# Optimization experiments

Measured on AMD Instinct MI355X. Metric: run time of the kernel, lower is better.

The kernel has to match this reference:

```python
import jax, jax.numpy as jnp
import numpy as np

NUM_HEADS = 16
BIG_NEG = -1e9  # additive mask value for padded keys (fp32)


def setup_inputs() -> dict:
    key = jax.random.key(0)
    ks = jax.random.split(key, 12)
    T, S, B, E = 2048, 2048, 2, 1024
    bound = np.sqrt(6.0 / (E + E))  # xavier_uniform for square E x E weights
    inp = {
        'query': jax.random.normal(ks[0], (T, B, E), jnp.float32),
        'key': jax.random.normal(ks[1], (S, B, E), jnp.float32),
        'value': jax.random.normal(ks[2], (S, B, E), jnp.float32),
        'attn_mask': jax.random.normal(ks[3], (T, S), jnp.float32) * 0.1,
        'key_padding_mask': jnp.zeros((B, S), dtype=bool),
        'Wq': jax.random.uniform(ks[4], (E, E), jnp.float32, -bound, bound),
        'bq': jnp.zeros((E,), jnp.float32),
        'Wk': jax.random.uniform(ks[5], (E, E), jnp.float32, -bound, bound),
        'bk': jnp.zeros((E,), jnp.float32),
        'Wv': jax.random.uniform(ks[6], (E, E), jnp.float32, -bound, bound),
        'bv': jnp.zeros((E,), jnp.float32),
        'Wo': jax.random.uniform(ks[7], (E, E), jnp.float32, -bound, bound),
        'bo': jnp.zeros((E,), jnp.float32),
    }
    return inp


def reference(query, key, value, attn_mask, key_padding_mask,
              Wq, bq, Wk, bk, Wv, bv, Wo, bo):
    T, B, E = query.shape
    S = key.shape[0]
    H = NUM_HEADS
    d = E // H
    scale = 1.0 / jnp.sqrt(jnp.asarray(d, query.dtype))

    # projections (nn.Linear: x @ W.T + b), then split heads
    q = (query @ Wq.T + bq).reshape(T, B, H, d) * scale  # [T,B,H,d]
    k = (key @ Wk.T + bk).reshape(S, B, H, d)            # [S,B,H,d]
    v = (value @ Wv.T + bv).reshape(S, B, H, d)          # [S,B,H,d]

    # QK^T scores: [B,H,T,S]
    scores = jnp.einsum('tbhd,sbhd->bhts', q, k)

    # merge masks: additive attn_mask + key_padding_mask (True -> -inf)
    merged = attn_mask[None, None, :, :] + jnp.where(
        key_padding_mask[:, None, None, :], BIG_NEG, 0.0).astype(scores.dtype)
    scores = scores + merged

    attn = jax.nn.softmax(scores, axis=-1)  # dropout p=0 -> identity

    out = jnp.einsum('bhts,sbhd->tbhd', attn, v).reshape(T, B, E)
    return out @ Wo.T + bo  # [T,B,E]
```

## Files before the change

kernel.cpp:

```cpp
#include <hip/hip_runtime.h>
#include <hip/hip_bf16.h>

typedef unsigned short u16;
typedef __attribute__((ext_vector_type(8))) short bf16x8;
typedef __attribute__((ext_vector_type(4))) float f32x4;

#define T_DIM 2048
#define S_DIM 2048
#define B_DIM 2
#define E_DIM 1024
#define H_DIM 16
#define D_HEAD 64
#define NTOK 4096

#if __has_builtin(__builtin_amdgcn_exp2f)
#define EXP2F(x) __builtin_amdgcn_exp2f(x)
#else
#define EXP2F(x) exp2f(x)
#endif

__device__ __forceinline__ float bf2f(u16 u) {
  union { unsigned int i; float f; } v; v.i = ((unsigned int)u) << 16; return v.f;
}
__device__ __forceinline__ u16 f2bf(float f) {
  union { float f; unsigned int i; } v; v.f = f;
  unsigned int r = v.i + 0x7fffu + ((v.i >> 16) & 1u);
  return (u16)(r >> 16);
}
__device__ __forceinline__ unsigned pk2(float a, float b) {
  return (unsigned)f2bf(a) | ((unsigned)f2bf(b) << 16);
}
__device__ __forceinline__ uint4 loadA8(const void* A, size_t base, int bf) {
  if (bf) return *(const uint4*)&((const u16*)A)[base];
  const float* af = (const float*)A + base;
  uint4 r;
  r.x = pk2(af[0], af[1]); r.y = pk2(af[2], af[3]);
  r.z = pk2(af[4], af[5]); r.w = pk2(af[6], af[7]);
  return r;
}

__global__ void detect_dtype(const u16* q, int* flag) {
  int lane = threadIdx.x;
  float v = bf2f(q[2 * lane]);
  bool ok = (v < 16.f) && (v > -16.f);
  unsigned long long b = __ballot(ok);
  if (lane == 0) *flag = (b == ~0ull) ? 1 : 0;
}

__global__ void prep_params(const void* Wq, const void* Wk, const void* Wv, const void* Wo,
                            const void* bq, const void* bk, const void* bv, const void* bo,
                            u16* wqkv, u16* wo, float* b3, float* bof,
                            const int* flag) {
  const int bf = *flag;
  const int W = E_DIM * E_DIM;
  int idx = blockIdx.x * 256 + threadIdx.x;
  if (idx < 4 * W) {
    int which = idx / W, i = idx - which * W;
    const void* src = which == 0 ? Wq : which == 1 ? Wk : which == 2 ? Wv : Wo;
    float v = bf ? bf2f(((const u16*)src)[i]) : ((const float*)src)[i];
    if (which == 0) v *= 0.125f;
    if (which < 3) wqkv[idx] = f2bf(v);
    else           wo[i] = f2bf(v);
  } else {
    int j = idx - 4 * W;
    if (j < 4 * E_DIM) {
      int which = j / E_DIM, i = j - which * E_DIM;
      const void* src = which == 0 ? bq : which == 1 ? bk : which == 2 ? bv : bo;
      float v = bf ? bf2f(((const u16*)src)[i]) : ((const float*)src)[i];
      if (which == 0) v *= 0.125f;
      if (which < 3) b3[j] = v;
      else           bof[i] = v;
    }
  }
}

__global__ void prep_mask(const void* mask, const unsigned char* kpm,
                          u16* Mc, const int* flag) {
  const float L2E = 1.44269504f;
  const int bf = *flag;
  size_t e8 = ((size_t)blockIdx.x * 256 + threadIdx.x) * 8;
  int b = (int)(e8 / ((size_t)T_DIM * S_DIM));
  size_t rem = e8 - (size_t)b * T_DIM * S_DIM;
  int t = (int)(rem / S_DIM), s = (int)(rem - (size_t)t * S_DIM);
  const unsigned char* kb = &kpm[(size_t)b * S_DIM + s];
  uint4 o;
  if (bf) {
    const u16* m8 = &((const u16*)mask)[(size_t)t * S_DIM + s];
    o.x = pk2((bf2f(m8[0]) + (kb[0] ? -1e9f : 0.f)) * L2E,
              (bf2f(m8[1]) + (kb[1] ? -1e9f : 0.f)) * L2E);
    o.y = pk2((bf2f(m8[2]) + (kb[2] ? -1e9f : 0.f)) * L2E,
              (bf2f(m8[3]) + (kb[3] ? -1e9f : 0.f)) * L2E);
    o.z = pk2((bf2f(m8[4]) + (kb[4] ? -1e9f : 0.f)) * L2E,
              (bf2f(m8[5]) + (kb[5] ? -1e9f : 0.f)) * L2E);
    o.w = pk2((bf2f(m8[6]) + (kb[6] ? -1e9f : 0.f)) * L2E,
              (bf2f(m8[7]) + (kb[7] ? -1e9f : 0.f)) * L2E);
  } else {
    const float* mf = (const float*)mask + (size_t)t * S_DIM + s;
    o.x = pk2((mf[0] + (kb[0] ? -1e9f : 0.f)) * L2E,
              (mf[1] + (kb[1] ? -1e9f : 0.f)) * L2E);
    o.y = pk2((mf[2] + (kb[2] ? -1e9f : 0.f)) * L2E,
              (mf[3] + (kb[3] ? -1e9f : 0.f)) * L2E);
    o.z = pk2((mf[4] + (kb[4] ? -1e9f : 0.f)) * L2E,
              (mf[5] + (kb[5] ? -1e9f : 0.f)) * L2E);
    o.w = pk2((mf[6] + (kb[6] ? -1e9f : 0.f)) * L2E,
              (mf[7] + (kb[7] ? -1e9f : 0.f)) * L2E);
  }
  *(uint4*)&Mc[e8] = o;
}

__launch_bounds__(256)
__global__ void transpose_v(const u16* __restrict__ vp, u16* __restrict__ vt) {
  __shared__ unsigned int t[64 * 65];
  const int tid = threadIdx.x;
  const int s0 = blockIdx.x * 64;
  const int bh = blockIdx.y;
  const int b = bh / H_DIM, h = bh % H_DIM;
  {
    int sr = tid >> 2, cq = (tid & 3) * 16;
    const u16* src = &vp[((size_t)(s0 + sr) * B_DIM + b) * E_DIM + h * 64 + cq];
#pragma unroll
    for (int j = 0; j < 16; j++) t[(cq + j) * 65 + sr] = src[j];
  }
  __syncthreads();
  {
    int d = tid >> 2, sq = (tid & 3) * 16;
    u16* dst = &vt[((size_t)bh * 64 + d) * S_DIM + s0 + sq];
    uint4 o0, o1;
    o0.x = (t[d*65+sq+0] & 0xffffu) | (t[d*65+sq+1] << 16);
    o0.y = (t[d*65+sq+2] & 0xffffu) | (t[d*65+sq+3] << 16);
    o0.z = (t[d*65+sq+4] & 0xffffu) | (t[d*65+sq+5] << 16);
    o0.w = (t[d*65+sq+6] & 0xffffu) | (t[d*65+sq+7] << 16);
    o1.x = (t[d*65+sq+8] & 0xffffu) | (t[d*65+sq+9] << 16);
    o1.y = (t[d*65+sq+10] & 0xffffu) | (t[d*65+sq+11] << 16);
    o1.z = (t[d*65+sq+12] & 0xffffu) | (t[d*65+sq+13] << 16);
    o1.w = (t[d*65+sq+14] & 0xffffu) | (t[d*65+sq+15] << 16);
    *(uint4*)&dst[0] = o0;
    *(uint4*)&dst[8] = o1;
  }
}

__launch_bounds__(256, 2)
__global__ void gemm_qkv(const void* __restrict__ Qi, const void* __restrict__ Ki,
                         const void* __restrict__ Vi, const u16* __restrict__ W3,
                         const float* __restrict__ b3,
                         u16* __restrict__ qp, u16* __restrict__ kp, u16* __restrict__ vp,
                         const int* __restrict__ flag) {
  __shared__ alignas(16) u16 As[128 * 72];
  __shared__ alignas(16) u16 Bs[128 * 72];
  const int bf = *flag;
  const int tid = threadIdx.x;
  const int wave = tid >> 6, lane = tid & 63;
  const int g = lane >> 4, c = lane & 15;
  const int wy = wave >> 1, wx = wave & 1;
  const int which = blockIdx.x >> 3;
  const void* A = which == 0 ? Qi : which == 1 ? Ki : Vi;
  u16* dst = which == 0 ? qp : which == 1 ? kp : vp;
  const int m0 = blockIdx.y * 128, n0 = blockIdx.x * 128;
  const int K = E_DIM;
  const int rr = tid >> 3, oo = (tid & 7) * 8;

  uint4 pa0, pa1, pa2, pa3, pb0, pb1, pb2, pb3;
  pa0 = loadA8(A, (size_t)(m0 + rr)      * K + oo, bf);
  pa1 = loadA8(A, (size_t)(m0 + rr + 32) * K + oo, bf);
  pa2 = loadA8(A, (size_t)(m0 + rr + 64) * K + oo, bf);
  pa3 = loadA8(A, (size_t)(m0 + rr + 96) * K + oo, bf);
  pb0 = *(const uint4*)&W3[(size_t)(n0 + rr)      * K + oo];
  pb1 = *(const uint4*)&W3[(size_t)(n0 + rr + 32) * K + oo];
  pb2 = *(const uint4*)&W3[(size_t)(n0 + rr + 64) * K + oo];
  pb3 = *(const uint4*)&W3[(size_t)(n0 + rr + 96) * K + oo];

  f32x4 acc[4][4] = {};
  for (int kc = 0; kc < K; kc += 64) {
    *(uint4*)&As[(rr)      * 72 + oo] = pa0;
    *(uint4*)&As[(rr + 32) * 72 + oo] = pa1;
    *(uint4*)&As[(rr + 64) * 72 + oo] = pa2;
    *(uint4*)&As[(rr + 96) * 72 + oo] = pa3;
    *(uint4*)&Bs[(rr)      * 72 + oo] = pb0;
    *(uint4*)&Bs[(rr + 32) * 72 + oo] = pb1;
    *(uint4*)&Bs[(rr + 64) * 72 + oo] = pb2;
    *(uint4*)&Bs[(rr + 96) * 72 + oo] = pb3;
    __syncthreads();
    if (kc + 64 < K) {
      int k2 = kc + 64;
      pa0 = loadA8(A, (size_t)(m0 + rr)      * K + k2 + oo, bf);
      pa1 = loadA8(A, (size_t)(m0 + rr + 32) * K + k2 + oo, bf);
      pa2 = loadA8(A, (size_t)(m0 + rr + 64) * K + k2 + oo, bf);
      pa3 = loadA8(A, (size_t)(m0 + rr + 96) * K + k2 + oo, bf);
      pb0 = *(const uint4*)&W3[(size_t)(n0 + rr)      * K + k2 + oo];
      pb1 = *(const uint4*)&W3[(size_t)(n0 + rr + 32) * K + k2 + oo];
      pb2 = *(const uint4*)&W3[(size_t)(n0 + rr + 64) * K + k2 + oo];
      pb3 = *(const uint4*)&W3[(size_t)(n0 + rr + 96) * K + k2 + oo];
    }
#pragma unroll
    for (int ks = 0; ks < 2; ks++) {
      bf16x8 av0 = *(const bf16x8*)&As[(wy * 64 + 0 * 16 + c) * 72 + ks * 32 + g * 8];
      bf16x8 av1 = *(const bf16x8*)&As[(wy * 64 + 1 * 16 + c) * 72 + ks * 32 + g * 8];
      bf16x8 av2 = *(const bf16x8*)&As[(wy * 64 + 2 * 16 + c) * 72 + ks * 32 + g * 8];
      bf16x8 av3 = *(const bf16x8*)&As[(wy * 64 + 3 * 16 + c) * 72 + ks * 32 + g * 8];
      bf16x8 bv0 = *(const bf16x8*)&Bs[(wx * 64 + 0 * 16 + c) * 72 + ks * 32 + g * 8];
      bf16x8 bv1 = *(const bf16x8*)&Bs[(wx * 64 + 1 * 16 + c) * 72 + ks * 32 + g * 8];
      bf16x8 bv2 = *(const bf16x8*)&Bs[(wx * 64 + 2 * 16 + c) * 72 + ks * 32 + g * 8];
      bf16x8 bv3 = *(const bf16x8*)&Bs[(wx * 64 + 3 * 16 + c) * 72 + ks * 32 + g * 8];
      acc[0][0] = __builtin_amdgcn_mfma_f32_16x16x32_bf16(av0, bv0, acc[0][0], 0, 0, 0);
      acc[0][1] = __builtin_amdgcn_mfma_f32_16x16x32_bf16(av0, bv1, acc[0][1], 0, 0, 0);
      acc[0][2] = __builtin_amdgcn_mfma_f32_16x16x32_bf16(av0, bv2, acc[0][2], 0, 0, 0);
      acc[0][3] = __builtin_amdgcn_mfma_f32_16x16x32_bf16(av0, bv3, acc[0][3], 0, 0, 0);
      acc[1][0] = __builtin_amdgcn_mfma_f32_16x16x32_bf16(av1, bv0, acc[1][0], 0, 0, 0);
      acc[1][1] = __builtin_amdgcn_mfma_f32_16x16x32_bf16(av1, bv1, acc[1][1], 0, 0, 0);
      acc[1][2] = __builtin_amdgcn_mfma_f32_16x16x32_bf16(av1, bv2, acc[1][2], 0, 0, 0);
      acc[1][3] = __builtin_amdgcn_mfma_f32_16x16x32_bf16(av1, bv3, acc[1][3], 0, 0, 0);
      acc[2][0] = __builtin_amdgcn_mfma_f32_16x16x32_bf16(av2, bv0, acc[2][0], 0, 0, 0);
      acc[2][1] = __builtin_amdgcn_mfma_f32_16x16x32_bf16(av2, bv1, acc[2][1], 0, 0, 0);
      acc[2][2] = __builtin_amdgcn_mfma_f32_16x16x32_bf16(av2, bv2, acc[2][2], 0, 0, 0);
      acc[2][3] = __builtin_amdgcn_mfma_f32_16x16x32_bf16(av2, bv3, acc[2][3], 0, 0, 0);
      acc[3][0] = __builtin_amdgcn_mfma_f32_16x16x32_bf16(av3, bv0, acc[3][0], 0, 0, 0);
      acc[3][1] = __builtin_amdgcn_mfma_f32_16x16x32_bf16(av3, bv1, acc[3][1], 0, 0, 0);
      acc[3][2] = __builtin_amdgcn_mfma_f32_16x16x32_bf16(av3, bv2, acc[3][2], 0, 0, 0);
      acc[3][3] = __builtin_amdgcn_mfma_f32_16x16x32_bf16(av3, bv3, acc[3][3], 0, 0, 0);
    }
    __syncthreads();
  }
#pragma unroll
  for (int mi = 0; mi < 4; mi++)
#pragma unroll
    for (int ni = 0; ni < 4; ni++)
#pragma unroll
      for (int r = 0; r < 4; r++) {
        int row = m0 + wy * 64 + mi * 16 + g * 4 + r;
        int col = n0 + wx * 64 + ni * 16 + c;
        int inner = col & (E_DIM - 1);
        dst[(size_t)row * E_DIM + inner] = f2bf(acc[mi][ni][r] + b3[col]);
      }
}

__launch_bounds__(256, 2)
__global__ void gemm_o(const u16* __restrict__ A, const u16* __restrict__ Bw,
                       const float* __restrict__ bias, void* __restrict__ C,
                       int out_f32) {
  __shared__ alignas(16) u16 As[64 * 72];
  __shared__ alignas(16) u16 Bs[128 * 72];
  const int tid = threadIdx.x;
  const int wave = tid >> 6, lane = tid & 63;
  const int g = lane >> 4, c = lane & 15;
  const int wy = wave >> 1, wx = wave & 1;
  const int m0 = blockIdx.y * 64, n0 = blockIdx.x * 128;
  const int K = E_DIM, N = E_DIM;
  const int rr = tid >> 3, oo = (tid & 7) * 8;

  uint4 pa0, pa1, pb0, pb1, pb2, pb3;
  pa0 = *(const uint4*)&A[(size_t)(m0 + rr)      * K + oo];
  pa1 = *(const uint4*)&A[(size_t)(m0 + rr + 32) * K + oo];
  pb0 = *(const uint4*)&Bw[(size_t)(n0 + rr)      * K + oo];
  pb1 = *(const uint4*)&Bw[(size_t)(n0 + rr + 32) * K + oo];
  pb2 = *(const uint4*)&Bw[(size_t)(n0 + rr + 64) * K + oo];
  pb3 = *(const uint4*)&Bw[(size_t)(n0 + rr + 96) * K + oo];

  f32x4 acc[2][4] = {};
  for (int kc = 0; kc < K; kc += 64) {
    *(uint4*)&As[(rr)      * 72 + oo] = pa0;
    *(uint4*)&As[(rr + 32) * 72 + oo] = pa1;
    *(uint4*)&Bs[(rr)      * 72 + oo] = pb0;
    *(uint4*)&Bs[(rr + 32) * 72 + oo] = pb1;
    *(uint4*)&Bs[(rr + 64) * 72 + oo] = pb2;
    *(uint4*)&Bs[(rr + 96) * 72 + oo] = pb3;
    __syncthreads();
    if (kc + 64 < K) {
      int k2 = kc + 64;
      pa0 = *(const uint4*)&A[(size_t)(m0 + rr)      * K + k2 + oo];
      pa1 = *(const uint4*)&A[(size_t)(m0 + rr + 32) * K + k2 + oo];
      pb0 = *(const uint4*)&Bw[(size_t)(n0 + rr)      * K + k2 + oo];
      pb1 = *(const uint4*)&Bw[(size_t)(n0 + rr + 32) * K + k2 + oo];
      pb2 = *(const uint4*)&Bw[(size_t)(n0 + rr + 64) * K + k2 + oo];
      pb3 = *(const uint4*)&Bw[(size_t)(n0 + rr + 96) * K + k2 + oo];
    }
#pragma unroll
    for (int ks = 0; ks < 2; ks++) {
      bf16x8 av0 = *(const bf16x8*)&As[(wy * 32 + 0 * 16 + c) * 72 + ks * 32 + g * 8];
      bf16x8 av1 = *(const bf16x8*)&As[(wy * 32 + 1 * 16 + c) * 72 + ks * 32 + g * 8];
      bf16x8 bv0 = *(const bf16x8*)&Bs[(wx * 64 + 0 * 16 + c) * 72 + ks * 32 + g * 8];
      bf16x8 bv1 = *(const bf16x8*)&Bs[(wx * 64 + 1 * 16 + c) * 72 + ks * 32 + g * 8];
      bf16x8 bv2 = *(const bf16x8*)&Bs[(wx * 64 + 2 * 16 + c) * 72 + ks * 32 + g * 8];
      bf16x8 bv3 = *(const bf16x8*)&Bs[(wx * 64 + 3 * 16 + c) * 72 + ks * 32 + g * 8];
      acc[0][0] = __builtin_amdgcn_mfma_f32_16x16x32_bf16(av0, bv0, acc[0][0], 0, 0, 0);
      acc[0][1] = __builtin_amdgcn_mfma_f32_16x16x32_bf16(av0, bv1, acc[0][1], 0, 0, 0);
      acc[0][2] = __builtin_amdgcn_mfma_f32_16x16x32_bf16(av0, bv2, acc[0][2], 0, 0, 0);
      acc[0][3] = __builtin_amdgcn_mfma_f32_16x16x32_bf16(av0, bv3, acc[0][3], 0, 0, 0);
      acc[1][0] = __builtin_amdgcn_mfma_f32_16x16x32_bf16(av1, bv0, acc[1][0], 0, 0, 0);
      acc[1][1] = __builtin_amdgcn_mfma_f32_16x16x32_bf16(av1, bv1, acc[1][1], 0, 0, 0);
      acc[1][2] = __builtin_amdgcn_mfma_f32_16x16x32_bf16(av1, bv2, acc[1][2], 0, 0, 0);
      acc[1][3] = __builtin_amdgcn_mfma_f32_16x16x32_bf16(av1, bv3, acc[1][3], 0, 0, 0);
    }
    __syncthreads();
  }
#pragma unroll
  for (int mi = 0; mi < 2; mi++)
#pragma unroll
    for (int ni = 0; ni < 4; ni++)
#pragma unroll
      for (int r = 0; r < 4; r++) {
        int row = m0 + wy * 32 + mi * 16 + g * 4 + r;
        int col = n0 + wx * 64 + ni * 16 + c;
        float v = acc[mi][ni][r] + bias[col];
        size_t idx = (size_t)row * N + col;
        if (out_f32) ((float*)C)[idx] = v;
        else         ((u16*)C)[idx] = f2bf(v);
      }
}

__launch_bounds__(256, 4)
__global__ void flash_attn(const u16* __restrict__ Qb, const u16* __restrict__ Kb,
                           const u16* __restrict__ Vtg, const u16* __restrict__ Mc,
                           u16* __restrict__ ctx) {
  __shared__ alignas(16) u16 Ks[64 * 72];
  __shared__ alignas(16) u16 Vs[64 * 72];
  __shared__ alignas(16) u16 MP[64 * 72];
  const int tid = threadIdx.x;
  const int wave = tid >> 6, lane = tid & 63;
  const int g = lane >> 4, c = lane & 15;
  const int bh = blockIdx.x;
  const int t0 = blockIdx.y * 64;
  const int b = bh / H_DIM, h = bh % H_DIM;
  const size_t hoff = (size_t)h * D_HEAD;
  const float L2E = 1.44269504f;
  const u16* mc = &Mc[((size_t)b * T_DIM + t0) * S_DIM];
  const int rr = tid >> 3, oo = (tid & 7) * 8;

  *(uint4*)&Ks[(rr)      * 72 + oo] =
      *(const uint4*)&Qb[((size_t)(t0 + rr)      * B_DIM + b) * E_DIM + hoff + oo];
  *(uint4*)&Ks[(rr + 32) * 72 + oo] =
      *(const uint4*)&Qb[((size_t)(t0 + rr + 32) * B_DIM + b) * E_DIM + hoff + oo];
  __syncthreads();
  const int arow = wave * 16 + c;
  bf16x8 q0 = *(const bf16x8*)&Ks[arow * 72 + g * 8];
  bf16x8 q1 = *(const bf16x8*)&Ks[arow * 72 + 32 + g * 8];

  uint4 pk0, pk1, pv0, pv1, pm0, pm1;
  pk0 = *(const uint4*)&Kb[((size_t)(rr)      * B_DIM + b) * E_DIM + hoff + oo];
  pk1 = *(const uint4*)&Kb[((size_t)(rr + 32) * B_DIM + b) * E_DIM + hoff + oo];
  pv0 = *(const uint4*)&Vtg[((size_t)bh * 64 + rr)      * S_DIM + oo];
  pv1 = *(const uint4*)&Vtg[((size_t)bh * 64 + rr + 32) * S_DIM + oo];
  pm0 = *(const uint4*)&mc[(size_t)(rr)      * S_DIM + oo];
  pm1 = *(const uint4*)&mc[(size_t)(rr + 32) * S_DIM + oo];
  __syncthreads();

  f32x4 O[4] = {};
  float rs[4] = {0.f, 0.f, 0.f, 0.f};

  for (int s0 = 0; s0 < S_DIM; s0 += 64) {
    *(uint4*)&Ks[(rr)      * 72 + oo] = pk0;
    *(uint4*)&Ks[(rr + 32) * 72 + oo] = pk1;
    *(uint4*)&Vs[(rr)      * 72 + oo] = pv0;
    *(uint4*)&Vs[(rr + 32) * 72 + oo] = pv1;
    *(uint4*)&MP[(rr)      * 72 + oo] = pm0;
    *(uint4*)&MP[(rr + 32) * 72 + oo] = pm1;
    __syncthreads();
    if (s0 + 64 < S_DIM) {
      int s2 = s0 + 64;
      pk0 = *(const uint4*)&Kb[((size_t)(s2 + rr)      * B_DIM + b) * E_DIM + hoff + oo];
      pk1 = *(const uint4*)&Kb[((size_t)(s2 + rr + 32) * B_DIM + b) * E_DIM + hoff + oo];
      pv0 = *(const uint4*)&Vtg[((size_t)bh * 64 + rr)      * S_DIM + s2 + oo];
      pv1 = *(const uint4*)&Vtg[((size_t)bh * 64 + rr + 32) * S_DIM + s2 + oo];
      pm0 = *(const uint4*)&mc[(size_t)(rr)      * S_DIM + s2 + oo];
      pm1 = *(const uint4*)&mc[(size_t)(rr + 32) * S_DIM + s2 + oo];
    }

    f32x4 sc[4] = {};
#pragma unroll
    for (int n = 0; n < 4; n++) {
      bf16x8 k0 = *(const bf16x8*)&Ks[(n * 16 + c) * 72 + g * 8];
      bf16x8 k1 = *(const bf16x8*)&Ks[(n * 16 + c) * 72 + 32 + g * 8];
      sc[n] = __builtin_amdgcn_mfma_f32_16x16x32_bf16(q0, k0, sc[n], 0, 0, 0);
      sc[n] = __builtin_amdgcn_mfma_f32_16x16x32_bf16(q1, k1, sc[n], 0, 0, 0);
    }
#pragma unroll
    for (int n = 0; n < 4; n++)
#pragma unroll
      for (int r = 0; r < 4; r++) {
        int a = (wave * 16 + g * 4 + r) * 72 + n * 16 + c;
        float pval = EXP2F(fmaf(sc[n][r], L2E, bf2f(MP[a])));
        rs[r] += pval;
        MP[a] = f2bf(pval);
      }
    bf16x8 p0 = *(const bf16x8*)&MP[arow * 72 + g * 8];
    bf16x8 p1 = *(const bf16x8*)&MP[arow * 72 + 32 + g * 8];
#pragma unroll
    for (int n = 0; n < 4; n++) {
      bf16x8 v0 = *(const bf16x8*)&Vs[(n * 16 + c) * 72 + g * 8];
      bf16x8 v1 = *(const bf16x8*)&Vs[(n * 16 + c) * 72 + 32 + g * 8];
      O[n] = __builtin_amdgcn_mfma_f32_16x16x32_bf16(p0, v0, O[n], 0, 0, 0);
      O[n] = __builtin_amdgcn_mfma_f32_16x16x32_bf16(p1, v1, O[n], 0, 0, 0);
    }
    __syncthreads();
  }
#pragma unroll
  for (int r = 0; r < 4; r++) {
    float l = rs[r];
#pragma unroll
    for (int off = 1; off < 16; off <<= 1) l += __shfl_xor(l, off, 64);
    float rl = 1.f / l;
    int t = t0 + wave * 16 + g * 4 + r;
#pragma unroll
    for (int n = 0; n < 4; n++) {
      int dcol = n * 16 + c;
      ctx[((size_t)t * B_DIM + b) * E_DIM + hoff + dcol] = f2bf(O[n][r] * rl);
    }
  }
}

extern "C" void kernel_launch(void* const* d_in, const int* in_sizes, int n_in,
                              void* d_out, int out_size, void* d_ws, size_t ws_size,
                              hipStream_t stream) {
  const void* query = d_in[0];
  const void* key   = d_in[1];
  const void* value = d_in[2];
  const void* amask = d_in[3];
  const unsigned char* kpm = (const unsigned char*)d_in[4];
  const void* Wq = d_in[5];  const void* bq = d_in[6];
  const void* Wk = d_in[7];  const void* bk = d_in[8];
  const void* Wv = d_in[9];  const void* bv = d_in[10];
  const void* Wo = d_in[11]; const void* bo = d_in[12];

  int out_f32 = 0;
  {
    hipDeviceptr_t base = nullptr; size_t sz = 0;
    if (hipMemGetAddressRange(&base, &sz, (hipDeviceptr_t)d_out) == hipSuccess && sz) {
      size_t avail = sz - (size_t)((char*)d_out - (char*)base);
      size_t need_f32 = (size_t)out_size * 4;
      if (avail >= need_f32 && avail <= need_f32 + need_f32 / 2) out_f32 = 1;
    }
  }

  char* ws = (char*)d_ws;
  size_t off = 0;
  auto alloc = [&](size_t bytes) {
    void* p = ws + off;
    off += (bytes + 255) & ~(size_t)255;
    return p;
  };
  int*   flag = (int*)  alloc(256);
  u16*   qp   = (u16*)  alloc((size_t)NTOK * E_DIM * 2);
  u16*   kp   = (u16*)  alloc((size_t)NTOK * E_DIM * 2);
  u16*   vp   = (u16*)  alloc((size_t)NTOK * E_DIM * 2);
  u16*   vt   = (u16*)  alloc((size_t)NTOK * E_DIM * 2);
  u16*   Mcb  = (u16*)  alloc((size_t)B_DIM * T_DIM * S_DIM * 2);
  u16*   wqkv = (u16*)  alloc((size_t)3 * E_DIM * E_DIM * 2);
  u16*   wo   = (u16*)  alloc((size_t)E_DIM * E_DIM * 2);
  float* b3   = (float*)alloc(3 * E_DIM * 4);
  float* bof  = (float*)alloc(E_DIM * 4);
  if (off > ws_size) return;

  detect_dtype<<<1, 64, 0, stream>>>((const u16*)query, flag);

  {
    int total = 4 * E_DIM * E_DIM + 4 * E_DIM;
    prep_params<<<(total + 255) / 256, 256, 0, stream>>>(
        Wq, Wk, Wv, Wo, bq, bk, bv, bo, wqkv, wo, b3, bof, flag);
  }
  {
    size_t total8 = (size_t)B_DIM * T_DIM * S_DIM / 8;
    prep_mask<<<(unsigned)(total8 / 256), 256, 0, stream>>>(amask, kpm, Mcb, flag);
  }

  gemm_qkv<<<dim3(3 * E_DIM / 128, NTOK / 128), 256, 0, stream>>>(
      query, key, value, wqkv, b3, qp, kp, vp, flag);

  transpose_v<<<dim3(S_DIM / 64, B_DIM * H_DIM), 256, 0, stream>>>(vp, vt);

  u16* ctx = vp;
  flash_attn<<<dim3(B_DIM * H_DIM, T_DIM / 64), 256, 0, stream>>>(qp, kp, vt, Mcb, ctx);

  gemm_o<<<dim3(E_DIM / 128, NTOK / 64), 256, 0, stream>>>(ctx, wo, bof, d_out, out_f32);
}
```

Measured before the change: 311.4 us.

## Split attention over key dimension per wave, keep P in registers, reduce O via LDS

Restructures the flash attention kernel so each wave owns a 16-key slice of every 64-key tile instead of 16 query rows. Scores are computed as K·Q^T, so the exponentiated probabilities stay in registers and feed the PV MFMA directly, with two key tiles processed per iteration. This removes the LDS round trip for the mask and P tiles. Partial output accumulators are summed across waves through LDS at the end, which raises register use (occupancy hint dropped from 4 to 3) and adds a cross-wave reduction step. Mask values are now read straight from global memory inside the softmax step.

Measured after the change: 442.2 us. +42.0%, slower.

```diff
diff --git a/kernel.cpp b/kernel.cpp
--- a/kernel.cpp
+++ b/kernel.cpp
@@ -29,6 +29,17 @@
 }
 __device__ __forceinline__ unsigned pk2(float a, float b) {
   return (unsigned)f2bf(a) | ((unsigned)f2bf(b) << 16);
+}
+__device__ __forceinline__ float bfu_lo(unsigned w) {
+  union { unsigned int i; float f; } v; v.i = w << 16; return v.f;
+}
+__device__ __forceinline__ float bfu_hi(unsigned w) {
+  union { unsigned int i; float f; } v; v.i = w & 0xffff0000u; return v.f;
+}
+__device__ __forceinline__ bf16x8 mk8(uint2 a, uint2 b) {
+  union { uint4 u; bf16x8 v; } x;
+  x.u = make_uint4(a.x, a.y, b.x, b.y);
+  return x.v;
 }
 __device__ __forceinline__ uint4 loadA8(const void* A, size_t base, int bf) {
   if (bf) return *(const uint4*)&((const u16*)A)[base];
@@ -307,13 +318,49 @@
       }
 }
 
-__launch_bounds__(256, 4)
+#define STAGE(VSB) do {                                                        \
+    *(uint4*)&Ks[(rr)      * 72 + oo] = pkA;                                   \
+    *(uint4*)&Ks[(rr + 32) * 72 + oo] = pkB;                                   \
+    *(uint4*)&(VSB)[(rr)      * 72 + oo] = pvA;                                \
+    *(uint4*)&(VSB)[(rr + 32) * 72 + oo] = pvB;                                \
+  } while (0)
+
+#define PREFETCH(S2) do {                                                      \
+    pkA = *(const uint4*)&Kb[((size_t)((S2) + rr)      * B_DIM + b) * E_DIM + hoff + oo]; \
+    pkB = *(const uint4*)&Kb[((size_t)((S2) + rr + 32) * B_DIM + b) * E_DIM + hoff + oo]; \
+    pvA = *(const uint4*)&Vtg[((size_t)bh * 64 + rr)      * S_DIM + (S2) + oo]; \
+    pvB = *(const uint4*)&Vtg[((size_t)bh * 64 + rr + 32) * S_DIM + (S2) + oo]; \
+  } while (0)
+
+#define QKSOFT(PB, S0) do {                                                    \
+    f32x4 sc[4] = {};                                                          \
+    bf16x8 kf0 = *(const bf16x8*)&Ks[w16c * 72 + g * 8];                       \
+    bf16x8 kf1 = *(const bf16x8*)&Ks[w16c * 72 + 32 + g * 8];                  \
+    _Pragma("unroll")                                                          \
+    for (int n = 0; n < 4; n++) {                                              \
+      sc[n] = __builtin_amdgcn_mfma_f32_16x16x32_bf16(kf0, q[n][0], sc[n], 0, 0, 0); \
+      sc[n] = __builtin_amdgcn_mfma_f32_16x16x32_bf16(kf1, q[n][1], sc[n], 0, 0, 0); \
+    }                                                                          \
+    _Pragma("unroll")                                                          \
+    for (int n = 0; n < 4; n++) {                                              \
+      uint2 mw = *(const uint2*)&mc[(size_t)(n * 16 + c) * S_DIM + (S0) + wS + g * 4]; \
+      float p0 = EXP2F(fmaf(sc[n][0], L2E, bfu_lo(mw.x)));                     \
+      float p1 = EXP2F(fmaf(sc[n][1], L2E, bfu_hi(mw.x)));                     \
+      float p2 = EXP2F(fmaf(sc[n][2], L2E, bfu_lo(mw.y)));                     \
+      float p3 = EXP2F(fmaf(sc[n][3], L2E, bfu_hi(mw.y)));                     \
+      rs[n] += (p0 + p1) + (p2 + p3);                                          \
+      PB[n] = make_uint2(pk2(p0, p1), pk2(p2, p3));                            \
+    }                                                                          \
+  } while (0)
+
+__launch_bounds__(256, 3)
 __global__ void flash_attn(const u16* __restrict__ Qb, const u16* __restrict__ Kb,
                            const u16* __restrict__ Vtg, const u16* __restrict__ Mc,
                            u16* __restrict__ ctx) {
-  __shared__ alignas(16) u16 Ks[64 * 72];
-  __shared__ alignas(16) u16 Vs[64 * 72];
-  __shared__ alignas(16) u16 MP[64 * 72];
+  __shared__ alignas(16) u16 SH[3 * 64 * 72];
+  u16* Ks  = SH;
+  u16* Vs0 = SH + 4608;
+  u16* Vs1 = SH + 2 * 4608;
   const int tid = threadIdx.x;
   const int wave = tid >> 6, lane = tid & 63;
   const int g = lane >> 4, c = lane & 15;
@@ -324,86 +371,85 @@
   const float L2E = 1.44269504f;
   const u16* mc = &Mc[((size_t)b * T_DIM + t0) * S_DIM];
   const int rr = tid >> 3, oo = (tid & 7) * 8;
+  const int w16c = wave * 16 + c;
+  const int wS   = wave * 16;
 
   *(uint4*)&Ks[(rr)      * 72 + oo] =
       *(const uint4*)&Qb[((size_t)(t0 + rr)      * B_DIM + b) * E_DIM + hoff + oo];
   *(uint4*)&Ks[(rr + 32) * 72 + oo] =
       *(const uint4*)&Qb[((size_t)(t0 + rr + 32) * B_DIM + b) * E_DIM + hoff + oo];
   __syncthreads();
-  const int arow = wave * 16 + c;
-  bf16x8 q0 = *(const bf16x8*)&Ks[arow * 72 + g * 8];
-  bf16x8 q1 = *(const bf16x8*)&Ks[arow * 72 + 32 + g * 8];
-
-  uint4 pk0, pk1, pv0, pv1, pm0, pm1;
-  pk0 = *(const uint4*)&Kb[((size_t)(rr)      * B_DIM + b) * E_DIM + hoff + oo];
-  pk1 = *(const uint4*)&Kb[((size_t)(rr + 32) * B_DIM + b) * E_DIM + hoff + oo];
-  pv0 = *(const uint4*)&Vtg[((size_t)bh * 64 + rr)      * S_DIM + oo];
-  pv1 = *(const uint4*)&Vtg[((size_t)bh * 64 + rr + 32) * S_DIM + oo];
-  pm0 = *(const uint4*)&mc[(size_t)(rr)      * S_DIM + oo];
-  pm1 = *(const uint4*)&mc[(size_t)(rr + 32) * S_DIM + oo];
+  bf16x8 q[4][2];
+#pragma unroll
+  for (int n = 0; n < 4; n++) {
+    q[n][0] = *(const bf16x8*)&Ks[(n * 16 + c) * 72 + g * 8];
+    q[n][1] = *(const bf16x8*)&Ks[(n * 16 + c) * 72 + 32 + g * 8];
+  }
+
+  uint4 pkA, pkB, pvA, pvB;
+  PREFETCH(0);
   __syncthreads();
 
-  f32x4 O[4] = {};
+  f32x4 o[4][4] = {};
   float rs[4] = {0.f, 0.f, 0.f, 0.f};
-
-  for (int s0 = 0; s0 < S_DIM; s0 += 64) {
-    *(uint4*)&Ks[(rr)      * 72 + oo] = pk0;
-    *(uint4*)&Ks[(rr + 32) * 72 + oo] = pk1;
-    *(uint4*)&Vs[(rr)      * 72 + oo] = pv0;
-    *(uint4*)&Vs[(rr + 32) * 72 + oo] = pv1;
-    *(uint4*)&MP[(rr)      * 72 + oo] = pm0;
-    *(uint4*)&MP[(rr + 32) * 72 + oo] = pm1;
-    __syncthreads();
-    if (s0 + 64 < S_DIM) {
-      int s2 = s0 + 64;
-      pk0 = *(const uint4*)&Kb[((size_t)(s2 + rr)      * B_DIM + b) * E_DIM + hoff + oo];
-      pk1 = *(const uint4*)&Kb[((size_t)(s2 + rr + 32) * B_DIM + b) * E_DIM + hoff + oo];
-      pv0 = *(const uint4*)&Vtg[((size_t)bh * 64 + rr)      * S_DIM + s2 + oo];
-      pv1 = *(const uint4*)&Vtg[((size_t)bh * 64 + rr + 32) * S_DIM + s2 + oo];
-      pm0 = *(const uint4*)&mc[(size_t)(rr)      * S_DIM + s2 + oo];
-      pm1 = *(const uint4*)&mc[(size_t)(rr + 32) * S_DIM + s2 + oo];
-    }
-
-    f32x4 sc[4] = {};
-#pragma unroll
-    for (int n = 0; n < 4; n++) {
-      bf16x8 k0 = *(const bf16x8*)&Ks[(n * 16 + c) * 72 + g * 8];
-      bf16x8 k1 = *(const bf16x8*)&Ks[(n * 16 + c) * 72 + 32 + g * 8];
-      sc[n] = __builtin_amdgcn_mfma_f32_16x16x32_bf16(q0, k0, sc[n], 0, 0, 0);
-      sc[n] = __builtin_amdgcn_mfma_f32_16x16x32_bf16(q1, k1, sc[n], 0, 0, 0);
-    }
+  uint2 pbA[4], pbB[4];
+
+  for (int s0 = 0; s0 < S_DIM; s0 += 128) {
+    STAGE(Vs0);
+    __syncthreads();
+    PREFETCH(s0 + 64);
+    QKSOFT(pbA, s0);
+    __syncthreads();
+    STAGE(Vs1);
+    __syncthreads();
+    if (s0 + 128 < S_DIM) PREFETCH(s0 + 128);
+    QKSOFT(pbB, s0 + 64);
+#pragma unroll
+    for (int m = 0; m < 4; m++) {
+      uint2 va0 = *(const uint2*)&Vs0[(m * 16 + c) * 72 + wS + g * 4];
+      uint2 vb0 = *(const uint2*)&Vs1[(m * 16 + c) * 72 + wS + g * 4];
+      bf16x8 va = mk8(va0, vb0);
+#pragma unroll
+      for (int n = 0; n < 4; n++)
+        o[m][n] = __builtin_amdgcn_mfma_f32_16x16x32_bf16(va, mk8(pbA[n], pbB[n]),
+                                                          o[m][n], 0, 0, 0);
+    }
+    __syncthreads();
+  }
+
+  float l[4];
+#pragma unroll
+  for (int n = 0; n < 4; n++) {
+    float x = rs[n];
+    x += __shfl_xor(x, 16, 64);
+    x += __shfl_xor(x, 32, 64);
+    l[n] = x;
+  }
+  float* R  = (float*)SH;
+  float* Rs = (float*)(SH + 2 * 4608);
+  if (lane < 16) {
+#pragma unroll
+    for (int n = 0; n < 4; n++) Rs[wave * 64 + n * 16 + c] = l[n];
+  }
+  const int tt = tid >> 2, d4 = (tid & 3) * 4;
+  u16* cp = &ctx[((size_t)(t0 + tt) * B_DIM + b) * E_DIM + hoff + d4];
+  float rl = 0.f;
+#pragma unroll
+  for (int m = 0; m < 4; m++) {
 #pragma unroll
     for (int n = 0; n < 4; n++)
-#pragma unroll
-      for (int r = 0; r < 4; r++) {
-        int a = (wave * 16 + g * 4 + r) * 72 + n * 16 + c;
-        float pval = EXP2F(fmaf(sc[n][r], L2E, bf2f(MP[a])));
-        rs[r] += pval;
-        MP[a] = f2bf(pval);
-      }
-    bf16x8 p0 = *(const bf16x8*)&MP[arow * 72 + g * 8];
-    bf16x8 p1 = *(const bf16x8*)&MP[arow * 72 + 32 + g * 8];
-#pragma unroll
-    for (int n = 0; n < 4; n++) {
-      bf16x8 v0 = *(const bf16x8*)&Vs[(n * 16 + c) * 72 + g * 8];
-      bf16x8 v1 = *(const bf16x8*)&Vs[(n * 16 + c) * 72 + 32 + g * 8];
-      O[n] = __builtin_amdgcn_mfma_f32_16x16x32_bf16(p0, v0, O[n], 0, 0, 0);
-      O[n] = __builtin_amdgcn_mfma_f32_16x16x32_bf16(p1, v1, O[n], 0, 0, 0);
-    }
-    __syncthreads();
-  }
-#pragma unroll
-  for (int r = 0; r < 4; r++) {
-    float l = rs[r];
-#pragma unroll
-    for (int off = 1; off < 16; off <<= 1) l += __shfl_xor(l, off, 64);
-    float rl = 1.f / l;
-    int t = t0 + wave * 16 + g * 4 + r;
-#pragma unroll
-    for (int n = 0; n < 4; n++) {
-      int dcol = n * 16 + c;
-      ctx[((size_t)t * B_DIM + b) * E_DIM + hoff + dcol] = f2bf(O[n][r] * rl);
-    }
+      *(f32x4*)&R[wave * 1024 + (n * 16 + c) * 16 + g * 4] = o[m][n];
+    __syncthreads();
+    if (m == 0)
+      rl = 1.f / (Rs[tt] + Rs[64 + tt] + Rs[128 + tt] + Rs[192 + tt]);
+    f32x4 v0 = *(const f32x4*)&R[tt * 16 + d4];
+    f32x4 v1 = *(const f32x4*)&R[1024 + tt * 16 + d4];
+    f32x4 v2 = *(const f32x4*)&R[2048 + tt * 16 + d4];
+    f32x4 v3 = *(const f32x4*)&R[3072 + tt * 16 + d4];
+    f32x4 s = (v0 + v1) + (v2 + v3);
+    *(uint2*)&cp[m * 16] = make_uint2(pk2(s[0] * rl, s[1] * rl),
+                                      pk2(s[2] * rl, s[3] * rl));
+    __syncthreads();
   }
 }
 
```
